# Kernel tuning notes

Measured on AMD Instinct MI355X. Metric: run time of the kernel, lower is better.

The kernel has to match this reference:

```python
import jax, jax.numpy as jnp
import numpy as np

D, NH, NL, NP, DFF = 256, 8, 4, 4, 1024
DH = D // NH
SHAPES = [(64, 64), (32, 32), (16, 16), (8, 8)]
LEN = sum(h * w for h, w in SHAPES)  # 5440
B = 4
EPS = 1e-5


def setup_inputs() -> dict:
    key = jax.random.key(0)
    ks = jax.random.split(key, 24)
    def lin_w(k, fin, fout, scale=None):
        s = (1.0 / np.sqrt(fin)) if scale is None else scale
        return jax.random.normal(k, (fin, fout), jnp.float32) * s
    def lin_b(k, fout, scale=0.01):
        return jax.random.normal(k, (fout,), jnp.float32) * scale
    inp = {
        'src': jax.random.normal(ks[0], (B, LEN, D), jnp.float32),
        'pos_lvl_embed': jax.random.normal(ks[1], (B, LEN, D), jnp.float32),
        'spatial_shapes': jnp.array(SHAPES, jnp.int32),
        'level_start_index': jnp.array(np.cumsum([0] + [h * w for h, w in SHAPES[:-1]]), jnp.int32),
        # MSDeformAttn params
        'Wv': lin_w(ks[2], D, D), 'bv': lin_b(ks[3], D),
        'Woff': lin_w(ks[4], D, NH * NL * NP * 2, scale=0.001),  # small offsets, like grid init
        'boff': jax.random.normal(ks[5], (NH * NL * NP * 2,), jnp.float32) * 0.5,
        'Wa': lin_w(ks[6], D, NH * NL * NP), 'ba': lin_b(ks[7], NH * NL * NP),
        'Wo': lin_w(ks[8], D, D), 'bo': lin_b(ks[9], D),
        # FFN params
        'W1': lin_w(ks[10], D, DFF), 'b1': lin_b(ks[11], DFF),
        'W2': lin_w(ks[12], DFF, D), 'b2': lin_b(ks[13], D),
        # LayerNorms
        'g1': jnp.ones((D,), jnp.float32), 'be1': jnp.zeros((D,), jnp.float32),
        'g2': jnp.ones((D,), jnp.float32), 'be2': jnp.zeros((D,), jnp.float32),
    }
    return inp


def _layernorm(x, g, b):
    mu = jnp.mean(x, axis=-1, keepdims=True)
    var = jnp.var(x, axis=-1, keepdims=True)
    return (x - mu) * jax.lax.rsqrt(var + EPS) * g + b


def _bilinear(v, x, y):
    # v: [B, H, W, NH, DH]; x, y: [B, Lq, NH, NP] pixel coords (align_corners=False, zero padding)
    Bv, H, W = v.shape[0], v.shape[1], v.shape[2]
    x0, y0 = jnp.floor(x), jnp.floor(y)
    bb = jnp.arange(Bv)[:, None, None, None]
    hh = jnp.arange(NH)[None, None, :, None]
    out = 0.0
    for dx in (0, 1):
        for dy in (0, 1):
            xi, yi = x0 + dx, y0 + dy
            w = (1.0 - jnp.abs(x - xi)) * (1.0 - jnp.abs(y - yi))
            valid = (xi >= 0) & (xi <= W - 1) & (yi >= 0) & (yi <= H - 1)
            xc = jnp.clip(xi, 0, W - 1).astype(jnp.int32)
            yc = jnp.clip(yi, 0, H - 1).astype(jnp.int32)
            out = out + v[bb, yc, xc, hh] * (w * valid)[..., None]
    return out  # [B, Lq, NH, NP, DH]


def _ms_deform_attn(query, value_flat, shapes, starts, Wv, bv, Woff, boff, Wa, ba, Wo, bo):
    Bq, Lq = query.shape[0], query.shape[1]
    # reference points: normalized center of each query's own spatial location (valid_ratios == 1)
    refs = []
    for (H, W) in shapes:
        gy, gx = jnp.meshgrid(jnp.arange(H, dtype=jnp.float32), jnp.arange(W, dtype=jnp.float32), indexing='ij')
        refs.append(jnp.stack([(gx + 0.5) / W, (gy + 0.5) / H], -1).reshape(-1, 2))
    ref = jnp.concatenate(refs, 0)  # [Len, 2] (x, y)

    value = (value_flat @ Wv + bv).reshape(Bq, Lq, NH, DH)
    off = (query @ Woff + boff).reshape(Bq, Lq, NH, NL, NP, 2)
    attn = jax.nn.softmax((query @ Wa + ba).reshape(Bq, Lq, NH, NL * NP), axis=-1).reshape(Bq, Lq, NH, NL, NP)
    norm = jnp.array([[w, h] for (h, w) in shapes], jnp.float32)  # [NL, 2] = (W, H)
    loc = ref[None, :, None, None, None, :] + off / norm[None, None, None, :, None, :]  # [B,Lq,NH,NL,NP,2]

    out = 0.0
    for l, (H, W) in enumerate(shapes):
        s = starts[l]
        v_l = value[:, s:s + H * W].reshape(Bq, H, W, NH, DH)
        x = loc[:, :, :, l, :, 0] * W - 0.5
        y = loc[:, :, :, l, :, 1] * H - 0.5
        sampled = _bilinear(v_l, x, y)  # [B,Lq,NH,NP,DH]
        out = out + jnp.sum(sampled * attn[:, :, :, l, :, None], axis=3)
    return out.reshape(Bq, Lq, D) @ Wo + bo


def reference(src, spatial_shapes, level_start_index, pos_lvl_embed,
              Wv, bv, Woff, boff, Wa, ba, Wo, bo,
              W1, b1, W2, b2, g1, be1, g2, be2):
    shapes = [(int(h), int(w)) for h, w in np.asarray(spatial_shapes)]  # static metadata
    starts = [int(s) for s in np.asarray(level_start_index)]
    src2 = _ms_deform_attn(src + pos_lvl_embed, src, shapes, starts, Wv, bv, Woff, boff, Wa, ba, Wo, bo)
    x = _layernorm(src + src2, g1, be1)
    ffn = jax.nn.relu(x @ W1 + b1) @ W2 + b2
    return _layernorm(x + ffn, g2, be2)
```

## Files before the change

kernel.cpp:

```cpp
#include <hip/hip_runtime.h>
#include <hip/hip_fp16.h>
#include <cstddef>
#include <cstdint>

#define DMODEL 256
#define NHEAD  8
#define NLVL   4
#define NPT    4
#define DHEAD  32
#define DFFN   1024
#define SLEN   5440
#define BATCH  4
#define NTOK   (BATCH * SLEN)
#define NT256  ((size_t)NTOK * 256)
#define GYR    170
#define GYP    176
#define LN_EPS 1e-5f

typedef __attribute__((ext_vector_type(4))) float f32x4;
typedef __attribute__((ext_vector_type(8))) short s16x8;

__device__ __forceinline__ unsigned short f2bf(float f) {
    union { float f; unsigned u; } v; v.f = f;
    unsigned u = v.u;
    u += 0x7FFFu + ((u >> 16) & 1u);
    return (unsigned short)(u >> 16);
}
__device__ __forceinline__ float bf2f(unsigned short h) {
    union { unsigned u; float f; } v; v.u = ((unsigned)h) << 16;
    return v.f;
}

__device__ __forceinline__ void g2l16(const unsigned short* g, unsigned short* l) {
    __builtin_amdgcn_global_load_lds(
        (const __attribute__((address_space(1))) unsigned int*)g,
        (__attribute__((address_space(3))) unsigned int*)l, 16, 0, 0);
}

__global__ __launch_bounds__(256) void prep_tr_kernel(
    const float* __restrict__ src, const float* __restrict__ pos,
    unsigned short* __restrict__ srcB, unsigned short* __restrict__ qB,
    const float* __restrict__ Wv, const float* __restrict__ Woff,
    const float* __restrict__ Wa, const float* __restrict__ Wo,
    const float* __restrict__ W1, const float* __restrict__ W2,
    unsigned short* __restrict__ WvT, unsigned short* __restrict__ WcatT,
    unsigned short* __restrict__ WoT,
    unsigned short* __restrict__ W1T, unsigned short* __restrict__ W2T)
{
    if (blockIdx.x < 5440) {
        const size_t i = ((size_t)blockIdx.x * 256 + threadIdx.x) * 4;
        const float4 s = *(const float4*)(src + i);
        const float4 p = *(const float4*)(pos + i);
        ushort4 sb, qb;
        sb.x = f2bf(s.x); sb.y = f2bf(s.y); sb.z = f2bf(s.z); sb.w = f2bf(s.w);
        qb.x = f2bf(s.x + p.x); qb.y = f2bf(s.y + p.y);
        qb.z = f2bf(s.z + p.z); qb.w = f2bf(s.w + p.w);
        *(ushort4*)(srcB + i) = sb;
        *(ushort4*)(qB + i) = qb;
        return;
    }
    const int bid = blockIdx.x - 5440;
    const float* W; unsigned short* Wt; int K, N, t;
    if (bid < 16)       { W = Wv;   Wt = WvT;              K = 256;  N = 256;  t = bid; }
    else if (bid < 32)  { W = Woff; Wt = WcatT;            K = 256;  N = 256;  t = bid - 16; }
    else if (bid < 40)  { W = Wa;   Wt = WcatT + 256*256;  K = 256;  N = 128;  t = bid - 32; }
    else if (bid < 56)  { W = Wo;   Wt = WoT;              K = 256;  N = 256;  t = bid - 40; }
    else if (bid < 120) { W = W1;   Wt = W1T;              K = 256;  N = 1024; t = bid - 56; }
    else                { W = W2;   Wt = W2T;              K = 1024; N = 256;  t = bid - 120; }
    const int ntx = N >> 6;
    const int k0 = (t / ntx) * 64, n0 = (t % ntx) * 64;

    __shared__ float T[64][65];
    const int r  = threadIdx.x >> 4;
    const int c4 = (threadIdx.x & 15) * 4;
    #pragma unroll
    for (int rep = 0; rep < 4; rep++) {
        const int k = rep * 16 + r;
        const float4 v = *(const float4*)(W + (size_t)(k0 + k) * N + n0 + c4);
        T[c4 + 0][k] = v.x; T[c4 + 1][k] = v.y;
        T[c4 + 2][k] = v.z; T[c4 + 3][k] = v.w;
    }
    __syncthreads();
    #pragma unroll
    for (int rep = 0; rep < 4; rep++) {
        const int n = rep * 16 + r;
        ushort4 o;
        o.x = f2bf(T[n][c4 + 0]); o.y = f2bf(T[n][c4 + 1]);
        o.z = f2bf(T[n][c4 + 2]); o.w = f2bf(T[n][c4 + 3]);
        *(ushort4*)(Wt + (size_t)(n0 + n) * K + k0 + c4) = o;
    }
}

template <int KK, int NXB, bool RELU, int OM>
__global__ __launch_bounds__(256, 2) void gemm_lds_kernel(
    const unsigned short* __restrict__ A,
    const unsigned short* __restrict__ Bt,
    const float* __restrict__ bias, const float* __restrict__ bias2,
    int bsplit,
    void* __restrict__ Cout, int N)
{
    const int lin = blockIdx.x;
    const int c8  = lin & 7;
    const int rr  = lin >> 3;
    const int bx  = rr % NXB;
    const int yy  = (rr / NXB) * 8 + c8;
    if (yy >= GYR) return;
    const int row0 = yy * 128;
    const int col0 = bx * 128;

    __shared__ __align__(16) unsigned short sA[128 * 64];
    __shared__ __align__(16) unsigned short sB[128 * 64];

    const int tid  = threadIdx.x;
    const int wid  = tid >> 6;
    const int lane = tid & 63;
    const int m16  = lane & 15;
    const int q    = lane >> 4;
    const int wr   = (wid >> 1) * 64;
    const int wc   = (wid & 1) * 64;

    const int srow = lane >> 3;
    const int schk = (lane & 7) ^ srow;

    f32x4 acc[4][4];
    #pragma unroll
    for (int m = 0; m < 4; m++)
        #pragma unroll
        for (int n = 0; n < 4; n++) acc[m][n] = (f32x4){0.f, 0.f, 0.f, 0.f};

    #pragma unroll 1
    for (int kt = 0; kt < KK / 64; kt++) {
        #pragma unroll
        for (int i = 0; i < 4; i++) {
            const int j = wid * 4 + i;
            const int r = j * 8 + srow;
            g2l16(A  + (size_t)(row0 + r) * KK + kt * 64 + schk * 8, &sA[j * 512]);
            g2l16(Bt + (size_t)(col0 + r) * KK + kt * 64 + schk * 8, &sB[j * 512]);
        }
        __syncthreads();

        #pragma unroll
        for (int ks = 0; ks < 2; ks++) {
            s16x8 a[4], b[4];
            #pragma unroll
            for (int m = 0; m < 4; m++) {
                const int r  = wr + m * 16 + m16;
                const int cc = (ks * 4 + q) ^ (r & 7);
                a[m] = *(const s16x8*)&sA[r * 64 + cc * 8];
            }
            #pragma unroll
            for (int n = 0; n < 4; n++) {
                const int r  = wc + n * 16 + m16;
                const int cc = (ks * 4 + q) ^ (r & 7);
                b[n] = *(const s16x8*)&sB[r * 64 + cc * 8];
            }
            #pragma unroll
            for (int m = 0; m < 4; m++)
                #pragma unroll
                for (int n = 0; n < 4; n++)
                    acc[m][n] = __builtin_amdgcn_mfma_f32_16x16x32_bf16(
                        a[m], b[n], acc[m][n], 0, 0, 0);
        }
        __syncthreads();
    }

    #pragma unroll
    for (int n = 0; n < 4; n++) {
        const int col  = col0 + wc + n * 16 + m16;
        const float bc = (col < bsplit) ? bias[col] : bias2[col - bsplit];
        #pragma unroll
        for (int m = 0; m < 4; m++) {
            #pragma unroll
            for (int r = 0; r < 4; r++) {
                const int row = row0 + wr + m * 16 + q * 4 + r;
                float v = acc[m][n][r] + bc;
                if (RELU) v = fmaxf(v, 0.f);
                if (OM == 1)
                    ((unsigned short*)Cout)[(size_t)row * N + col] = f2bf(v);
                else if (OM == 2)
                    ((__half*)Cout)[(size_t)row * N + col] = __float2half(v);
                else
                    ((float*)Cout)[(size_t)row * N + col] = v;
            }
        }
    }
}

__global__ __launch_bounds__(256) void msda_meta_kernel(
    const float* __restrict__ olg, uint4* __restrict__ meta)
{
    const int t  = blockIdx.x * 256 + threadIdx.x;
    const int p  = t & 15;
    const int h  = (t >> 4) & 7;
    const int bq = t >> 7;
    const int b  = bq / SLEN;
    const int q  = bq - b * SLEN;

    int rem, Wq;
    if (q < 4096)      { rem = q;        Wq = 64; }
    else if (q < 5120) { rem = q - 4096; Wq = 32; }
    else if (q < 5376) { rem = q - 5120; Wq = 16; }
    else               { rem = q - 5376; Wq = 8;  }
    const int gy = rem / Wq;
    const int gx = rem - gy * Wq;
    const float ref_x = (gx + 0.5f) / (float)Wq;
    const float ref_y = (gy + 0.5f) / (float)Wq;

    const float lg = olg[(size_t)bq * 384 + 256 + h * 16 + p];
    float mx = lg;
    #pragma unroll
    for (int m = 1; m < 16; m <<= 1) mx = fmaxf(mx, __shfl_xor(mx, m));
    const float e = expf(lg - mx);
    float s = e;
    #pragma unroll
    for (int m = 1; m < 16; m <<= 1) s += __shfl_xor(s, m);
    const float aw = e / s;

    const float2 o2 = *(const float2*)(olg + (size_t)bq * 384 + h * 32 + 2 * p);

    const int l = p >> 2;
    constexpr int LW[4] = {64, 32, 16, 8};
    constexpr int LS[4] = {0, 4096, 5120, 5376};
    const int Wl = LW[l];
    const float fW = (float)Wl;

    const float X = (ref_x + o2.x / fW) * fW - 0.5f;
    const float Y = (ref_y + o2.y / fW) * fW - 0.5f;
    const float x0f = floorf(X), y0f = floorf(Y);
    const float fx = X - x0f, fy = Y - y0f;
    const int x0 = (int)x0f, y0 = (int)y0f;

    unsigned idx[4]; __half hw[4];
    #pragma unroll
    for (int dy = 0; dy < 2; dy++) {
        const int yi = y0 + dy;
        const float wy = dy ? fy : (1.f - fy);
        const bool vy = (yi >= 0) && (yi < Wl);
        const int yc = min(max(yi, 0), Wl - 1);
        #pragma unroll
        for (int dx = 0; dx < 2; dx++) {
            const int xi = x0 + dx;
            const float wx = dx ? fx : (1.f - fx);
            const bool vx = (xi >= 0) && (xi < Wl);
            const int xc = min(max(xi, 0), Wl - 1);
            const int c = dy * 2 + dx;
            idx[c] = (unsigned)(LS[l] + yc * Wl + xc);
            hw[c] = __float2half((vx && vy) ? (aw * wx * wy) : 0.f);
        }
    }
    union { __half2 h2; unsigned u; } pk0, pk1;
    pk0.h2 = __halves2half2(hw[0], hw[1]);
    pk1.h2 = __halves2half2(hw[2], hw[3]);
    uint4 m;
    m.x = idx[0] | (idx[1] << 16);
    m.y = idx[2] | (idx[3] << 16);
    m.z = pk0.u;
    m.w = pk1.u;
    meta[((size_t)bq * 16 + p) * 8 + h] = m;
}

__global__ __launch_bounds__(256) void msda_sample_kernel(
    const __half* __restrict__ value, const uint4* __restrict__ meta,
    unsigned short* __restrict__ out)
{
    const int lin = blockIdx.x;
    const int c8  = lin & 7;
    const int rr  = lin >> 3;
    const int b   = c8 >> 1;
    const int i8  = (c8 & 1) + 2 * rr;

    const int tid = threadIdx.x;
    const int sub = tid & 3;
    const int h   = (tid >> 2) & 7;
    const int t8  = tid >> 5;
    const int bq  = b * SLEN + i8 * 8 + t8;

    const char* vb = (const char*)value + (size_t)b * SLEN * 512;
    const unsigned laneoff = (unsigned)(h * 64 + sub * 16);
    const uint4* metap = meta + (size_t)bq * 128 + h;

    __half2 acc[4][4];
    #pragma unroll
    for (int i = 0; i < 4; i++)
        #pragma unroll
        for (int k = 0; k < 4; k++)
            acc[i][k] = __float2half2_rn(0.f);

    for (int g = 0; g < 4; g++) {
        #pragma unroll
        for (int pp = 0; pp < 4; pp++) {
            const int p = g * 4 + pp;
            const uint4 m = metap[p * 8];
            const unsigned a0 = ((m.x & 0xFFFFu) << 9) + laneoff;
            const unsigned a1 = ((m.x >> 16) << 9) + laneoff;
            const unsigned a2 = ((m.y & 0xFFFFu) << 9) + laneoff;
            const unsigned a3 = ((m.y >> 16) << 9) + laneoff;
            const int4 v0 = *(const int4*)(vb + a0);
            const int4 v1 = *(const int4*)(vb + a1);
            const int4 v2 = *(const int4*)(vb + a2);
            const int4 v3 = *(const int4*)(vb + a3);
            union { unsigned u; __half2 h2; } wz, ww;
            wz.u = m.z; ww.u = m.w;
            const __half2 ws0 = __half2half2(__low2half(wz.h2));
            const __half2 ws1 = __half2half2(__high2half(wz.h2));
            const __half2 ws2 = __half2half2(__low2half(ww.h2));
            const __half2 ws3 = __half2half2(__high2half(ww.h2));
            const __half2* p0 = (const __half2*)&v0;
            const __half2* p1 = (const __half2*)&v1;
            const __half2* p2 = (const __half2*)&v2;
            const __half2* p3 = (const __half2*)&v3;
            #pragma unroll
            for (int k = 0; k < 4; k++) {
                acc[pp][k] = __hfma2(ws0, p0[k], acc[pp][k]);
                acc[pp][k] = __hfma2(ws1, p1[k], acc[pp][k]);
                acc[pp][k] = __hfma2(ws2, p2[k], acc[pp][k]);
                acc[pp][k] = __hfma2(ws3, p3[k], acc[pp][k]);
            }
        }
    }

    uint4 o;
    unsigned* ou = &o.x;
    #pragma unroll
    for (int k = 0; k < 4; k++) {
        float2 s = {0.f, 0.f};
        #pragma unroll
        for (int i = 0; i < 4; i++) {
            const float2 f = __half22float2(acc[i][k]);
            s.x += f.x; s.y += f.y;
        }
        ou[k] = (unsigned)f2bf(s.x) | ((unsigned)f2bf(s.y) << 16);
    }
    *(uint4*)(out + (size_t)bq * 256 + h * 32 + sub * 8) = o;
}

template <bool X1B, bool X2B, bool WF, bool WB>
__global__ __launch_bounds__(256) void ln_kernel(
    const void* __restrict__ x1, const void* __restrict__ x2,
    const float* __restrict__ g, const float* __restrict__ be,
    float* __restrict__ outf, unsigned short* __restrict__ outb)
{
    const int lane = threadIdx.x & 63;
    const int wid  = threadIdx.x >> 6;
    const size_t row  = (size_t)blockIdx.x * 4 + wid;
    const size_t base = row * 256 + lane * 4;

    float a0, a1, a2, a3, b0, b1, b2, b3;
    if (X1B) {
        const ushort4 a = *(const ushort4*)((const unsigned short*)x1 + base);
        a0 = bf2f(a.x); a1 = bf2f(a.y); a2 = bf2f(a.z); a3 = bf2f(a.w);
    } else {
        const float4 a = *(const float4*)((const float*)x1 + base);
        a0 = a.x; a1 = a.y; a2 = a.z; a3 = a.w;
    }
    if (X2B) {
        const ushort4 b = *(const ushort4*)((const unsigned short*)x2 + base);
        b0 = bf2f(b.x); b1 = bf2f(b.y); b2 = bf2f(b.z); b3 = bf2f(b.w);
    } else {
        const float4 b = *(const float4*)((const float*)x2 + base);
        b0 = b.x; b1 = b.y; b2 = b.z; b3 = b.w;
    }
    const float v0 = a0 + b0, v1 = a1 + b1, v2 = a2 + b2, v3 = a3 + b3;

    float s  = v0 + v1 + v2 + v3;
    float s2 = v0 * v0 + v1 * v1 + v2 * v2 + v3 * v3;
    #pragma unroll
    for (int o = 32; o > 0; o >>= 1) {
        s  += __shfl_xor(s, o);
        s2 += __shfl_xor(s2, o);
    }
    const float mu  = s * (1.f / 256.f);
    const float var = s2 * (1.f / 256.f) - mu * mu;
    const float r   = rsqrtf(var + LN_EPS);

    const float4 gv = *(const float4*)(g  + lane * 4);
    const float4 bv = *(const float4*)(be + lane * 4);
    float4 o4;
    o4.x = (v0 - mu) * r * gv.x + bv.x;
    o4.y = (v1 - mu) * r * gv.y + bv.y;
    o4.z = (v2 - mu) * r * gv.z + bv.z;
    o4.w = (v3 - mu) * r * gv.w + bv.w;
    if (WF) *(float4*)(outf + base) = o4;
    if (WB) {
        ushort4 ob;
        ob.x = f2bf(o4.x); ob.y = f2bf(o4.y); ob.z = f2bf(o4.z); ob.w = f2bf(o4.w);
        *(ushort4*)(outb + base) = ob;
    }
}

extern "C" void kernel_launch(void* const* d_in, const int* in_sizes, int n_in,
                              void* d_out, int out_size, void* d_ws, size_t ws_size,
                              hipStream_t stream)
{
    const float* src  = (const float*)d_in[0];
    const float* pos  = (const float*)d_in[1];
    const float* Wv   = (const float*)d_in[4];
    const float* bv   = (const float*)d_in[5];
    const float* Woff = (const float*)d_in[6];
    const float* boff = (const float*)d_in[7];
    const float* Wa   = (const float*)d_in[8];
    const float* ba   = (const float*)d_in[9];
    const float* Wo   = (const float*)d_in[10];
    const float* bo   = (const float*)d_in[11];
    const float* W1   = (const float*)d_in[12];
    const float* b1   = (const float*)d_in[13];
    const float* W2   = (const float*)d_in[14];
    const float* b2   = (const float*)d_in[15];
    const float* g1   = (const float*)d_in[16];
    const float* be1  = (const float*)d_in[17];
    const float* g2   = (const float*)d_in[18];
    const float* be2  = (const float*)d_in[19];
    float* out = (float*)d_out;

    char* wsp = (char*)d_ws;
    unsigned short* srcB = (unsigned short*)wsp; wsp += NT256 * 2;
    unsigned short* qB   = (unsigned short*)wsp; wsp += NT256 * 2;
    unsigned short* tbufB = srcB;
    __half*         valB = (__half*)wsp;         wsp += NT256 * 2;
    float*          olg  = (float*)wsp;          wsp += (size_t)NTOK * 384 * 4;
    float*          src2 = olg;
    unsigned short* aoB  = (unsigned short*)wsp; wsp += NT256 * 2;
    unsigned short* xB   = (unsigned short*)wsp; wsp += NT256 * 2;
    unsigned short* h    = (unsigned short*)wsp; wsp += (size_t)NTOK * 1024 * 2;
    uint4*          meta = (uint4*)h;
    unsigned short* WvT  = (unsigned short*)wsp; wsp += 256 * 256 * 2;
    unsigned short* WcatT= (unsigned short*)wsp; wsp += 384 * 256 * 2;
    unsigned short* WoT  = (unsigned short*)wsp; wsp += 256 * 256 * 2;
    unsigned short* W1T  = (unsigned short*)wsp; wsp += 1024 * 256 * 2;
    unsigned short* W2T  = (unsigned short*)wsp; wsp += 256 * 1024 * 2;

    const dim3 blk(256);

    prep_tr_kernel<<<dim3(5624), blk, 0, stream>>>(
        src, pos, srcB, qB, Wv, Woff, Wa, Wo, W1, W2,
        WvT, WcatT, WoT, W1T, W2T);

    gemm_lds_kernel<256, 2, false, 2><<<dim3(2 * GYP), blk, 0, stream>>>(
        srcB, WvT, bv, bv, 1 << 30, valB, 256);
    gemm_lds_kernel<256, 3, false, 0><<<dim3(3 * GYP), blk, 0, stream>>>(
        qB, WcatT, boff, ba, 256, olg, 384);
    msda_meta_kernel<<<dim3(NTOK * 128 / 256), blk, 0, stream>>>(olg, meta);
    msda_sample_kernel<<<dim3(NTOK / 8), blk, 0, stream>>>(valB, meta, aoB);
    gemm_lds_kernel<256, 2, false, 0><<<dim3(2 * GYP), blk, 0, stream>>>(
        aoB, WoT, bo, bo, 1 << 30, src2, 256);
    ln_kernel<false, false, false, true><<<dim3(NTOK / 4), blk, 0, stream>>>(
        src, src2, g1, be1, nullptr, xB);
    gemm_lds_kernel<256, 8, true, 1><<<dim3(8 * GYP), blk, 0, stream>>>(
        xB, W1T, b1, b1, 1 << 30, h, 1024);
    gemm_lds_kernel<1024, 2, false, 1><<<dim3(2 * GYP), blk, 0, stream>>>(
        h, W2T, b2, b2, 1 << 30, tbufB, 256);
    ln_kernel<true, true, true, false><<<dim3(NTOK / 4), blk, 0, stream>>>(
        xB, tbufB, g2, be2, out, nullptr);
}
```

Before: 257.1 us.

## Fuse MSDA metadata computation into sampling kernel and double-buffer GEMM LDS tiles

```diff
diff --git a/kernel.cpp b/kernel.cpp
--- a/kernel.cpp
+++ b/kernel.cpp
@@ -108,8 +108,8 @@
     const int row0 = yy * 128;
     const int col0 = bx * 128;
 
-    __shared__ __align__(16) unsigned short sA[128 * 64];
-    __shared__ __align__(16) unsigned short sB[128 * 64];
+    __shared__ __align__(16) unsigned short sA[2][128 * 64];
+    __shared__ __align__(16) unsigned short sB[2][128 * 64];
 
     const int tid  = threadIdx.x;
     const int wid  = tid >> 6;
@@ -122,22 +122,32 @@
     const int srow = lane >> 3;
     const int schk = (lane & 7) ^ srow;
 
-    f32x4 acc[4][4];
-    #pragma unroll
-    for (int m = 0; m < 4; m++)
-        #pragma unroll
-        for (int n = 0; n < 4; n++) acc[m][n] = (f32x4){0.f, 0.f, 0.f, 0.f};
-
-    #pragma unroll 1
-    for (int kt = 0; kt < KK / 64; kt++) {
+    auto stage = [&](int buf, int kt) {
         #pragma unroll
         for (int i = 0; i < 4; i++) {
             const int j = wid * 4 + i;
             const int r = j * 8 + srow;
-            g2l16(A  + (size_t)(row0 + r) * KK + kt * 64 + schk * 8, &sA[j * 512]);
-            g2l16(Bt + (size_t)(col0 + r) * KK + kt * 64 + schk * 8, &sB[j * 512]);
-        }
-        __syncthreads();
+            g2l16(A  + (size_t)(row0 + r) * KK + kt * 64 + schk * 8,
+                  &sA[buf][j * 512]);
+            g2l16(Bt + (size_t)(col0 + r) * KK + kt * 64 + schk * 8,
+                  &sB[buf][j * 512]);
+        }
+    };
+
+    f32x4 acc[4][4];
+    #pragma unroll
+    for (int m = 0; m < 4; m++)
+        #pragma unroll
+        for (int n = 0; n < 4; n++) acc[m][n] = (f32x4){0.f, 0.f, 0.f, 0.f};
+
+    constexpr int NT = KK / 64;
+    stage(0, 0);
+    __syncthreads();
+
+    #pragma unroll 1
+    for (int kt = 0; kt < NT; kt++) {
+        const int cur = kt & 1;
+        if (kt + 1 < NT) stage(cur ^ 1, kt + 1);
 
         #pragma unroll
         for (int ks = 0; ks < 2; ks++) {
@@ -146,13 +156,13 @@
             for (int m = 0; m < 4; m++) {
                 const int r  = wr + m * 16 + m16;
                 const int cc = (ks * 4 + q) ^ (r & 7);
-                a[m] = *(const s16x8*)&sA[r * 64 + cc * 8];
+                a[m] = *(const s16x8*)&sA[cur][r * 64 + cc * 8];
             }
             #pragma unroll
             for (int n = 0; n < 4; n++) {
                 const int r  = wc + n * 16 + m16;
                 const int cc = (ks * 4 + q) ^ (r & 7);
-                b[n] = *(const s16x8*)&sB[r * 64 + cc * 8];
+                b[n] = *(const s16x8*)&sB[cur][r * 64 + cc * 8];
             }
             #pragma unroll
             for (int m = 0; m < 4; m++)
@@ -186,81 +196,8 @@
     }
 }
 
-__global__ __launch_bounds__(256) void msda_meta_kernel(
-    const float* __restrict__ olg, uint4* __restrict__ meta)
-{
-    const int t  = blockIdx.x * 256 + threadIdx.x;
-    const int p  = t & 15;
-    const int h  = (t >> 4) & 7;
-    const int bq = t >> 7;
-    const int b  = bq / SLEN;
-    const int q  = bq - b * SLEN;
-
-    int rem, Wq;
-    if (q < 4096)      { rem = q;        Wq = 64; }
-    else if (q < 5120) { rem = q - 4096; Wq = 32; }
-    else if (q < 5376) { rem = q - 5120; Wq = 16; }
-    else               { rem = q - 5376; Wq = 8;  }
-    const int gy = rem / Wq;
-    const int gx = rem - gy * Wq;
-    const float ref_x = (gx + 0.5f) / (float)Wq;
-    const float ref_y = (gy + 0.5f) / (float)Wq;
-
-    const float lg = olg[(size_t)bq * 384 + 256 + h * 16 + p];
-    float mx = lg;
-    #pragma unroll
-    for (int m = 1; m < 16; m <<= 1) mx = fmaxf(mx, __shfl_xor(mx, m));
-    const float e = expf(lg - mx);
-    float s = e;
-    #pragma unroll
-    for (int m = 1; m < 16; m <<= 1) s += __shfl_xor(s, m);
-    const float aw = e / s;
-
-    const float2 o2 = *(const float2*)(olg + (size_t)bq * 384 + h * 32 + 2 * p);
-
-    const int l = p >> 2;
-    constexpr int LW[4] = {64, 32, 16, 8};
-    constexpr int LS[4] = {0, 4096, 5120, 5376};
-    const int Wl = LW[l];
-    const float fW = (float)Wl;
-
-    const float X = (ref_x + o2.x / fW) * fW - 0.5f;
-    const float Y = (ref_y + o2.y / fW) * fW - 0.5f;
-    const float x0f = floorf(X), y0f = floorf(Y);
-    const float fx = X - x0f, fy = Y - y0f;
-    const int x0 = (int)x0f, y0 = (int)y0f;
-
-    unsigned idx[4]; __half hw[4];
-    #pragma unroll
-    for (int dy = 0; dy < 2; dy++) {
-        const int yi = y0 + dy;
-        const float wy = dy ? fy : (1.f - fy);
-        const bool vy = (yi >= 0) && (yi < Wl);
-        const int yc = min(max(yi, 0), Wl - 1);
-        #pragma unroll
-        for (int dx = 0; dx < 2; dx++) {
-            const int xi = x0 + dx;
-            const float wx = dx ? fx : (1.f - fx);
-            const bool vx = (xi >= 0) && (xi < Wl);
-            const int xc = min(max(xi, 0), Wl - 1);
-            const int c = dy * 2 + dx;
-            idx[c] = (unsigned)(LS[l] + yc * Wl + xc);
-            hw[c] = __float2half((vx && vy) ? (aw * wx * wy) : 0.f);
-        }
-    }
-    union { __half2 h2; unsigned u; } pk0, pk1;
-    pk0.h2 = __halves2half2(hw[0], hw[1]);
-    pk1.h2 = __halves2half2(hw[2], hw[3]);
-    uint4 m;
-    m.x = idx[0] | (idx[1] << 16);
-    m.y = idx[2] | (idx[3] << 16);
-    m.z = pk0.u;
-    m.w = pk1.u;
-    meta[((size_t)bq * 16 + p) * 8 + h] = m;
-}
-
 __global__ __launch_bounds__(256) void msda_sample_kernel(
-    const __half* __restrict__ value, const uint4* __restrict__ meta,
+    const __half* __restrict__ value, const float* __restrict__ olg,
     unsigned short* __restrict__ out)
 {
     const int lin = blockIdx.x;
@@ -273,11 +210,87 @@
     const int sub = tid & 3;
     const int h   = (tid >> 2) & 7;
     const int t8  = tid >> 5;
-    const int bq  = b * SLEN + i8 * 8 + t8;
+    const int q   = i8 * 8 + t8;
+    const int bq  = b * SLEN + q;
+
+    __shared__ __align__(16) uint4 smeta[8 * 16 * 8];
+
+    {
+        int rem, Wq;
+        if (q < 4096)      { rem = q;        Wq = 64; }
+        else if (q < 5120) { rem = q - 4096; Wq = 32; }
+        else if (q < 5376) { rem = q - 5120; Wq = 16; }
+        else               { rem = q - 5376; Wq = 8;  }
+        const int gy = rem / Wq;
+        const int gx = rem - gy * Wq;
+        const float ref_x = (gx + 0.5f) / (float)Wq;
+        const float ref_y = (gy + 0.5f) / (float)Wq;
+
+        const float4 lgv = *(const float4*)(olg + (size_t)bq * 384 + 256 + h * 16 + sub * 4);
+        float mx = fmaxf(fmaxf(lgv.x, lgv.y), fmaxf(lgv.z, lgv.w));
+        mx = fmaxf(mx, __shfl_xor(mx, 1));
+        mx = fmaxf(mx, __shfl_xor(mx, 2));
+        float e0 = expf(lgv.x - mx), e1 = expf(lgv.y - mx);
+        float e2 = expf(lgv.z - mx), e3 = expf(lgv.w - mx);
+        float s = e0 + e1 + e2 + e3;
+        s += __shfl_xor(s, 1);
+        s += __shfl_xor(s, 2);
+        const float inv_s = 1.f / s;
+
+        const float4 o01 = *(const float4*)(olg + (size_t)bq * 384 + h * 32 + sub * 8);
+        const float4 o23 = *(const float4*)(olg + (size_t)bq * 384 + h * 32 + sub * 8 + 4);
+
+        constexpr int LW[4] = {64, 32, 16, 8};
+        constexpr int LS[4] = {0, 4096, 5120, 5376};
+        const int Wl = LW[sub];
+        const float fW = (float)Wl;
+        const float ew[4] = {e0, e1, e2, e3};
+        const float ox[4] = {o01.x, o01.z, o23.x, o23.z};
+        const float oy[4] = {o01.y, o01.w, o23.y, o23.w};
+
+        #pragma unroll
+        for (int j = 0; j < 4; j++) {
+            const float aw = ew[j] * inv_s;
+            const float X = (ref_x + ox[j] / fW) * fW - 0.5f;
+            const float Y = (ref_y + oy[j] / fW) * fW - 0.5f;
+            const float x0f = floorf(X), y0f = floorf(Y);
+            const float fx = X - x0f, fy = Y - y0f;
+            const int x0 = (int)x0f, y0 = (int)y0f;
+
+            unsigned idx[4]; __half hw[4];
+            #pragma unroll
+            for (int dy = 0; dy < 2; dy++) {
+                const int yi = y0 + dy;
+                const float wy = dy ? fy : (1.f - fy);
+                const bool vy = (yi >= 0) && (yi < Wl);
+                const int yc = min(max(yi, 0), Wl - 1);
+                #pragma unroll
+                for (int dx = 0; dx < 2; dx++) {
+                    const int xi = x0 + dx;
+                    const float wx = dx ? fx : (1.f - fx);
+                    const bool vx = (xi >= 0) && (xi < Wl);
+                    const int xc = min(max(xi, 0), Wl - 1);
+                    const int c = dy * 2 + dx;
+                    idx[c] = (unsigned)(LS[sub] + yc * Wl + xc);
+                    hw[c] = __float2half((vx && vy) ? (aw * wx * wy) : 0.f);
+                }
+            }
+            union { __half2 h2; unsigned u; } pk0, pk1;
+            pk0.h2 = __halves2half2(hw[0], hw[1]);
+            pk1.h2 = __halves2half2(hw[2], hw[3]);
+            uint4 m;
+            m.x = idx[0] | (idx[1] << 16);
+            m.y = idx[2] | (idx[3] << 16);
+            m.z = pk0.u;
+            m.w = pk1.u;
+            smeta[((t8 * 16) + sub * 4 + j) * 8 + h] = m;
+        }
+    }
+    __syncthreads();
 
     const char* vb = (const char*)value + (size_t)b * SLEN * 512;
     const unsigned laneoff = (unsigned)(h * 64 + sub * 16);
-    const uint4* metap = meta + (size_t)bq * 128 + h;
+    const uint4* metap = &smeta[(t8 * 16) * 8 + h];
 
     __half2 acc[4][4];
     #pragma unroll
@@ -422,7 +435,6 @@
     unsigned short* aoB  = (unsigned short*)wsp; wsp += NT256 * 2;
     unsigned short* xB   = (unsigned short*)wsp; wsp += NT256 * 2;
     unsigned short* h    = (unsigned short*)wsp; wsp += (size_t)NTOK * 1024 * 2;
-    uint4*          meta = (uint4*)h;
     unsigned short* WvT  = (unsigned short*)wsp; wsp += 256 * 256 * 2;
     unsigned short* WcatT= (unsigned short*)wsp; wsp += 384 * 256 * 2;
     unsigned short* WoT  = (unsigned short*)wsp; wsp += 256 * 256 * 2;
@@ -439,8 +451,7 @@
         srcB, WvT, bv, bv, 1 << 30, valB, 256);
     gemm_lds_kernel<256, 3, false, 0><<<dim3(3 * GYP), blk, 0, stream>>>(
         qB, WcatT, boff, ba, 256, olg, 384);
-    msda_meta_kernel<<<dim3(NTOK * 128 / 256), blk, 0, stream>>>(olg, meta);
-    msda_sample_kernel<<<dim3(NTOK / 8), blk, 0, stream>>>(valB, meta, aoB);
+    msda_sample_kernel<<<dim3(NTOK / 8), blk, 0, stream>>>(valB, olg, aoB);
     gemm_lds_kernel<256, 2, false, 0><<<dim3(2 * GYP), blk, 0, stream>>>(
         aoB, WoT, bo, bo, 1 << 30, src2, 256);
     ln_kernel<false, false, false, true><<<dim3(NTOK / 4), blk, 0, stream>>>(
```

New measurement: 246.7 us. -4.1%, faster.
